# Kernel optimization log

Hardware: AMD Instinct MI355X
Metric: run time of the kernel (lower is better)

Reference implementation:

```python
import jax, jax.numpy as jnp
import numpy as np

N, E, G = 50000, 800000, 100
H, C = 4, 64


def _gatv2(x, src, dst, ea, Wl, bl, Wr, br, We, att, bias):
    # PyG GATv2Conv: x_l = lin_l(x) (source side), x_r = lin_r(x) (target side)
    xl = (x @ Wl + bl).reshape(-1, H, C)
    xr = (x @ Wr + br).reshape(-1, H, C)
    e = (ea @ We).reshape(-1, H, C)               # [E,H,C]
    m = jax.nn.leaky_relu(xl[src] + xr[dst] + e, negative_slope=0.2)
    alpha = jnp.einsum('ehc,hc->eh', m, att)      # [E,H]
    amax = jax.ops.segment_max(alpha, dst, num_segments=N)
    amax = jnp.where(jnp.isfinite(amax), amax, jnp.float32(0.0))
    ex = jnp.exp(alpha - amax[dst])
    denom = jax.ops.segment_sum(ex, dst, num_segments=N)
    a = ex / (denom[dst] + jnp.float32(1e-16))    # segment softmax over in-edges
    out = jax.ops.segment_sum(xl[src] * a[..., None], dst, num_segments=N)
    return out.reshape(N, H * C) + bias


def setup_inputs() -> dict:
    key = jax.random.key(0)
    ks = jax.random.split(key, 24)
    lin = lambda k, i, o: (jax.random.normal(k, (i, o), jnp.float32) / np.sqrt(i).astype(np.float32))
    x = jax.random.normal(ks[0], (N, 8), jnp.float32)
    edge_index = jnp.stack([jax.random.randint(ks[1], (E,), 0, N),
                            jax.random.randint(ks[2], (E,), 0, N)])
    edge_attr = jax.random.normal(ks[3], (E, 1), jnp.float32)
    batch = jnp.sort(jax.random.randint(ks[4], (N,), 0, G))
    return dict(
        x=x, edge_index=edge_index, edge_attr=edge_attr, batch=batch,
        enc_W=lin(ks[5], 8, 64), enc_b=jnp.zeros((64,), jnp.float32),
        g1_Wl=lin(ks[6], 64, 256), g1_bl=jnp.zeros((256,), jnp.float32),
        g1_Wr=lin(ks[7], 64, 256), g1_br=jnp.zeros((256,), jnp.float32),
        g1_We=lin(ks[8], 1, 256),
        g1_att=jax.random.normal(ks[9], (H, C), jnp.float32) / np.sqrt(C).astype(np.float32),
        g1_bias=jnp.zeros((256,), jnp.float32),
        g2_Wl=lin(ks[10], 256, 256), g2_bl=jnp.zeros((256,), jnp.float32),
        g2_Wr=lin(ks[11], 256, 256), g2_br=jnp.zeros((256,), jnp.float32),
        g2_We=lin(ks[12], 1, 256),
        g2_att=jax.random.normal(ks[13], (H, C), jnp.float32) / np.sqrt(C).astype(np.float32),
        g2_bias=jnp.zeros((256,), jnp.float32),
        p1_W=lin(ks[14], 256, 128), p1_b=jnp.zeros((128,), jnp.float32),
        ln_g=jnp.ones((128,), jnp.float32), ln_b=jnp.zeros((128,), jnp.float32),
        p2_W=lin(ks[15], 128, 64), p2_b=jnp.zeros((64,), jnp.float32),
    )


def reference(x, edge_index, edge_attr, batch,
              enc_W, enc_b,
              g1_Wl, g1_bl, g1_Wr, g1_br, g1_We, g1_att, g1_bias,
              g2_Wl, g2_bl, g2_Wr, g2_br, g2_We, g2_att, g2_bias,
              p1_W, p1_b, ln_g, ln_b, p2_W, p2_b):
    src, dst = edge_index[0], edge_index[1]
    h = jax.nn.relu(x @ enc_W + enc_b)
    h = jax.nn.relu(_gatv2(h, src, dst, edge_attr, g1_Wl, g1_bl, g1_Wr, g1_br, g1_We, g1_att, g1_bias))
    h = jax.nn.relu(_gatv2(h, src, dst, edge_attr, g2_Wl, g2_bl, g2_Wr, g2_br, g2_We, g2_att, g2_bias))
    # global mean pool over graphs
    sums = jax.ops.segment_sum(h, batch, num_segments=G)
    cnt = jax.ops.segment_sum(jnp.ones((N, 1), h.dtype), batch, num_segments=G)
    p = sums / jnp.maximum(cnt, jnp.float32(1.0))
    # post MLP (dropout is identity in eval)
    z = p @ p1_W + p1_b
    mu = jnp.mean(z, axis=-1, keepdims=True)
    var = jnp.mean(jnp.square(z - mu), axis=-1, keepdims=True)
    z = (z - mu) * jax.lax.rsqrt(var + jnp.float32(1e-5)) * ln_g + ln_b
    z = jax.nn.relu(z)
    return jax.nn.relu(z @ p2_W + p2_b)
```

## Files before the change

kernel.cpp:

```cpp
#include <hip/hip_runtime.h>

#define NH 4
#define CH 64

__global__ void encoder_kernel(const float* __restrict__ x, const float* __restrict__ W,
                               const float* __restrict__ b, float* __restrict__ h, int N) {
  int idx = blockIdx.x * blockDim.x + threadIdx.x;
  if (idx >= N * 64) return;
  int n = idx >> 6, j = idx & 63;
  const float* xp = x + n * 8;
  float acc = b[j];
#pragma unroll
  for (int k = 0; k < 8; ++k) acc = fmaf(xp[k], W[k * 64 + j], acc);
  h[idx] = fmaxf(acc, 0.0f);
}

template <int K>
__global__ void lin_lr_kernel(const float* __restrict__ h,
                              const float* __restrict__ Wl, const float* __restrict__ bl,
                              const float* __restrict__ Wr, const float* __restrict__ br,
                              float* __restrict__ xl, float* __restrict__ xr, int N) {
  __shared__ float hs[8][K];
  int n0 = blockIdx.x * 8;
  int j = threadIdx.x;
  int nmax = N - n0; if (nmax > 8) nmax = 8;
  for (int idx = j; idx < nmax * K; idx += 256) {
    int m = idx / K, k = idx % K;
    hs[m][k] = h[(size_t)(n0 + m) * K + k];
  }
  __syncthreads();
  float accl[8], accr[8];
  float bjl = bl[j], bjr = br[j];
#pragma unroll
  for (int m = 0; m < 8; ++m) { accl[m] = bjl; accr[m] = bjr; }
  for (int k = 0; k < K; ++k) {
    float wl = Wl[k * 256 + j];
    float wr = Wr[k * 256 + j];
#pragma unroll
    for (int m = 0; m < 8; ++m) {
      accl[m] = fmaf(hs[m][k], wl, accl[m]);
      accr[m] = fmaf(hs[m][k], wr, accr[m]);
    }
  }
  for (int m = 0; m < nmax; ++m) {
    xl[(size_t)(n0 + m) * 256 + j] = accl[m];
    xr[(size_t)(n0 + m) * 256 + j] = accr[m];
  }
}

__global__ void hist_kernel(const int* __restrict__ dst, int* __restrict__ deg, int E) {
  int e = blockIdx.x * blockDim.x + threadIdx.x;
  if (e < E) atomicAdd(&deg[dst[e]], 1);
}

__global__ void scan_partial_kernel(const int* __restrict__ deg, int* __restrict__ partial, int N) {
  __shared__ int sm[256];
  int t = threadIdx.x;
  int i = blockIdx.x * 256 + t;
  sm[t] = (i < N) ? deg[i] : 0;
  __syncthreads();
#pragma unroll
  for (int s = 128; s > 0; s >>= 1) {
    if (t < s) sm[t] += sm[t + s];
    __syncthreads();
  }
  if (t == 0) partial[blockIdx.x] = sm[0];
}

__global__ void scan_offsets_kernel(int* __restrict__ partial, int nb) {
  __shared__ int sm[256];
  int t = threadIdx.x;
  int v = (t < nb) ? partial[t] : 0;
  sm[t] = v;
  __syncthreads();
#pragma unroll
  for (int off = 1; off < 256; off <<= 1) {
    int a = (t >= off) ? sm[t - off] : 0;
    __syncthreads();
    sm[t] += a;
    __syncthreads();
  }
  if (t < nb) partial[t] = sm[t] - v;
}

__global__ void scan_final_kernel(const int* __restrict__ deg, const int* __restrict__ partial,
                                  int* __restrict__ rowptr, int* __restrict__ cursor, int N, int E) {
  __shared__ int sm[256];
  int t = threadIdx.x;
  int i = blockIdx.x * 256 + t;
  int v = (i < N) ? deg[i] : 0;
  sm[t] = v;
  __syncthreads();
#pragma unroll
  for (int off = 1; off < 256; off <<= 1) {
    int a = (t >= off) ? sm[t - off] : 0;
    __syncthreads();
    sm[t] += a;
    __syncthreads();
  }
  if (i < N) {
    int ex = partial[blockIdx.x] + sm[t] - v;
    rowptr[i] = ex;
    cursor[i] = ex;
  }
  if (i == 0) rowptr[N] = E;
}

__global__ void scatter_build_kernel(const int* __restrict__ src, const int* __restrict__ dst,
                                     const float* __restrict__ ea, int* __restrict__ cursor,
                                     int* __restrict__ srcs, float* __restrict__ eas, int E) {
  int e = blockIdx.x * blockDim.x + threadIdx.x;
  if (e >= E) return;
  int d = dst[e];
  int pos = atomicAdd(&cursor[d], 1);
  srcs[pos] = src[e];
  eas[pos] = ea[e];
}

__device__ __forceinline__ void edge_accum(const float4 xlv, const float eav,
                                           const float4 xr4, const float4 We4, const float4 at4,
                                           float4& acc, float& denom) {
  float4 v;
  v.x = fmaf(eav, We4.x, xlv.x + xr4.x);
  v.y = fmaf(eav, We4.y, xlv.y + xr4.y);
  v.z = fmaf(eav, We4.z, xlv.z + xr4.z);
  v.w = fmaf(eav, We4.w, xlv.w + xr4.w);
  v.x = (v.x >= 0.f) ? v.x : 0.2f * v.x;
  v.y = (v.y >= 0.f) ? v.y : 0.2f * v.y;
  v.z = (v.z >= 0.f) ? v.z : 0.2f * v.z;
  v.w = (v.w >= 0.f) ? v.w : 0.2f * v.w;
  float p = v.x * at4.x + v.y * at4.y + v.z * at4.z + v.w * at4.w;
  p += __shfl_xor(p, 1, 64);
  p += __shfl_xor(p, 2, 64);
  p += __shfl_xor(p, 4, 64);
  p += __shfl_xor(p, 8, 64);
  float ex = __expf(p);
  denom += ex;
  acc.x = fmaf(ex, xlv.x, acc.x);
  acc.y = fmaf(ex, xlv.y, acc.y);
  acc.z = fmaf(ex, xlv.z, acc.z);
  acc.w = fmaf(ex, xlv.w, acc.w);
}

template <bool POOL>
__global__ void gat_aggregate_kernel(const int* __restrict__ rowptr,
                                     const int* __restrict__ srcs,
                                     const float* __restrict__ eas,
                                     const float* __restrict__ xl,
                                     const float* __restrict__ xr,
                                     const float* __restrict__ We,
                                     const float* __restrict__ att,
                                     const float* __restrict__ bias,
                                     float* __restrict__ out,
                                     const int* __restrict__ batch,
                                     float* __restrict__ sums,
                                     float* __restrict__ cnt,
                                     int N) {
  int d = (int)((blockIdx.x * (size_t)blockDim.x + threadIdx.x) >> 6);
  int lane = threadIdx.x & 63;
  if (d >= N) return;
  const float4* xl4p = (const float4*)xl;
  float4 xr4 = ((const float4*)xr)[(size_t)d * 64 + lane];
  float4 We4 = ((const float4*)We)[lane];
  float4 at4 = ((const float4*)att)[lane];
  int beg = rowptr[d], end = rowptr[d + 1];
  float4 acc = {0.f, 0.f, 0.f, 0.f};
  float denom = 0.f;
  int i = beg;
  for (; i + 3 < end; i += 4) {
    int s0 = srcs[i], s1 = srcs[i + 1], s2 = srcs[i + 2], s3 = srcs[i + 3];
    float e0 = eas[i], e1 = eas[i + 1], e2 = eas[i + 2], e3 = eas[i + 3];
    float4 a0 = xl4p[(size_t)s0 * 64 + lane];
    float4 a1 = xl4p[(size_t)s1 * 64 + lane];
    float4 a2 = xl4p[(size_t)s2 * 64 + lane];
    float4 a3 = xl4p[(size_t)s3 * 64 + lane];
    edge_accum(a0, e0, xr4, We4, at4, acc, denom);
    edge_accum(a1, e1, xr4, We4, at4, acc, denom);
    edge_accum(a2, e2, xr4, We4, at4, acc, denom);
    edge_accum(a3, e3, xr4, We4, at4, acc, denom);
  }
  for (; i < end; ++i) {
    int s0 = srcs[i];
    float e0 = eas[i];
    float4 a0 = xl4p[(size_t)s0 * 64 + lane];
    edge_accum(a0, e0, xr4, We4, at4, acc, denom);
  }
  float inv = 1.f / (denom + 1e-16f);
  float4 b4 = ((const float4*)bias)[lane];
  float4 o;
  o.x = fmaxf(fmaf(acc.x, inv, b4.x), 0.f);
  o.y = fmaxf(fmaf(acc.y, inv, b4.y), 0.f);
  o.z = fmaxf(fmaf(acc.z, inv, b4.z), 0.f);
  o.w = fmaxf(fmaf(acc.w, inv, b4.w), 0.f);
  if (POOL) {
    int g = batch[d];
    float* sg = sums + (size_t)g * 256 + lane * 4;
    atomicAdd(sg + 0, o.x);
    atomicAdd(sg + 1, o.y);
    atomicAdd(sg + 2, o.z);
    atomicAdd(sg + 3, o.w);
    if (lane == 0) atomicAdd(&cnt[g], 1.0f);
  } else {
    ((float4*)out)[(size_t)d * 64 + lane] = o;
  }
}

__global__ void mlp_kernel(const float* __restrict__ sums, const float* __restrict__ cnt,
                           const float* __restrict__ p1W, const float* __restrict__ p1b,
                           const float* __restrict__ lng, const float* __restrict__ lnb,
                           const float* __restrict__ p2W, const float* __restrict__ p2b,
                           float* __restrict__ outp, int G) {
  __shared__ float p[256];
  __shared__ float z[128];
  __shared__ float wsum[2];
  __shared__ float wsum2[2];
  int g = blockIdx.x;
  int t = threadIdx.x;
  float c = fmaxf(cnt[g], 1.0f);
  p[t] = sums[(size_t)g * 256 + t] / c;
  p[t + 128] = sums[(size_t)g * 256 + t + 128] / c;
  __syncthreads();
  float acc = p1b[t];
  for (int k = 0; k < 256; ++k) acc = fmaf(p[k], p1W[k * 128 + t], acc);
  float v = acc;
#pragma unroll
  for (int off = 32; off > 0; off >>= 1) v += __shfl_xor(v, off, 64);
  if ((t & 63) == 0) wsum[t >> 6] = v;
  __syncthreads();
  float mu = (wsum[0] + wsum[1]) * (1.0f / 128.0f);
  float dv = acc - mu;
  float vv = dv * dv;
#pragma unroll
  for (int off = 32; off > 0; off >>= 1) vv += __shfl_xor(vv, off, 64);
  if ((t & 63) == 0) wsum2[t >> 6] = vv;
  __syncthreads();
  float var = (wsum2[0] + wsum2[1]) * (1.0f / 128.0f);
  float zv = dv * rsqrtf(var + 1e-5f) * lng[t] + lnb[t];
  z[t] = fmaxf(zv, 0.0f);
  __syncthreads();
  if (t < 64) {
    float o = p2b[t];
    for (int k = 0; k < 128; ++k) o = fmaf(z[k], p2W[k * 64 + t], o);
    outp[(size_t)g * 64 + t] = fmaxf(o, 0.0f);
  }
}

extern "C" void kernel_launch(void* const* d_in, const int* in_sizes, int n_in,
                              void* d_out, int out_size, void* d_ws, size_t ws_size,
                              hipStream_t stream) {
  const float* x      = (const float*)d_in[0];
  const int*   ei     = (const int*)d_in[1];
  const float* ea     = (const float*)d_in[2];
  const int*   batch  = (const int*)d_in[3];
  const float* enc_W  = (const float*)d_in[4];
  const float* enc_b  = (const float*)d_in[5];
  const float* Wl1    = (const float*)d_in[6];
  const float* bl1    = (const float*)d_in[7];
  const float* Wr1    = (const float*)d_in[8];
  const float* br1    = (const float*)d_in[9];
  const float* We1    = (const float*)d_in[10];
  const float* att1   = (const float*)d_in[11];
  const float* bias1  = (const float*)d_in[12];
  const float* Wl2    = (const float*)d_in[13];
  const float* bl2    = (const float*)d_in[14];
  const float* Wr2    = (const float*)d_in[15];
  const float* br2    = (const float*)d_in[16];
  const float* We2    = (const float*)d_in[17];
  const float* att2   = (const float*)d_in[18];
  const float* bias2  = (const float*)d_in[19];
  const float* p1W    = (const float*)d_in[20];
  const float* p1b    = (const float*)d_in[21];
  const float* lng    = (const float*)d_in[22];
  const float* lnb    = (const float*)d_in[23];
  const float* p2W    = (const float*)d_in[24];
  const float* p2b    = (const float*)d_in[25];
  float* outp = (float*)d_out;

  int N = in_sizes[0] / 8;
  int E = in_sizes[2];
  int G = out_size / 64;
  const int* src = ei;
  const int* dst = ei + E;
  int nb = (N + 255) / 256;

  float* ws      = (float*)d_ws;
  float* h0      = ws;
  float* B0      = h0     + (size_t)N * 64;
  float* B1      = B0     + (size_t)N * 256;
  float* B2      = B1     + (size_t)N * 256;
  float* eas     = B2     + (size_t)N * 256;
  float* sums    = eas    + (size_t)E;
  float* cnt     = sums   + (size_t)G * 256;
  int*   srcs    = (int*)(cnt + G);
  int*   rowptr  = srcs + (size_t)E;
  int*   cursor  = rowptr + (size_t)(N + 1);
  int*   partial = cursor + (size_t)N;

  encoder_kernel<<<(N * 64 + 255) / 256, 256, 0, stream>>>(x, enc_W, enc_b, h0, N);

  hipMemsetAsync(cursor, 0, (size_t)N * sizeof(int), stream);
  hist_kernel<<<(E + 255) / 256, 256, 0, stream>>>(dst, cursor, E);
  scan_partial_kernel<<<nb, 256, 0, stream>>>(cursor, partial, N);
  scan_offsets_kernel<<<1, 256, 0, stream>>>(partial, nb);
  scan_final_kernel<<<nb, 256, 0, stream>>>(cursor, partial, rowptr, cursor, N, E);
  scatter_build_kernel<<<(E + 255) / 256, 256, 0, stream>>>(src, dst, ea, cursor, srcs, eas, E);

  lin_lr_kernel<64><<<(N + 7) / 8, 256, 0, stream>>>(h0, Wl1, bl1, Wr1, br1, B0, B1, N);
  gat_aggregate_kernel<false><<<(N + 3) / 4, 256, 0, stream>>>(
      rowptr, srcs, eas, B0, B1, We1, att1, bias1, B2, nullptr, nullptr, nullptr, N);

  lin_lr_kernel<256><<<(N + 7) / 8, 256, 0, stream>>>(B2, Wl2, bl2, Wr2, br2, B0, B1, N);
  hipMemsetAsync(sums, 0, ((size_t)G * 256 + G) * sizeof(float), stream);
  gat_aggregate_kernel<true><<<(N + 3) / 4, 256, 0, stream>>>(
      rowptr, srcs, eas, B0, B1, We2, att2, bias2, nullptr, batch, sums, cnt, N);

  mlp_kernel<<<G, 128, 0, stream>>>(sums, cnt, p1W, p1b, lng, lnb, p2W, p2b, outp, G);
}
```

Baseline: 1.039 ms.

## Split GAT aggregation across edges and heads with one block per node

The aggregate kernel now launches one 256-thread block per destination node instead of one wavefront per node. Each wavefront owns one head, and its 64 lanes split into four edge slots of 16 channel lanes each. A node's in-edges are processed 16 at a time with masked tails, and the four slots are combined by cross-lane shuffles before output or pooling. This is meant to expose more parallel gather loads per node and shorten each node's serial edge loop, at the cost of wasted masked lanes on low-degree nodes and an extra shuffle reduction.

```diff
diff --git a/kernel.cpp b/kernel.cpp
--- a/kernel.cpp
+++ b/kernel.cpp
@@ -117,7 +117,7 @@
   eas[pos] = ea[e];
 }
 
-__device__ __forceinline__ void edge_accum(const float4 xlv, const float eav,
+__device__ __forceinline__ void edge_accum(const float4 xlv, const float eav, const float vmask,
                                            const float4 xr4, const float4 We4, const float4 at4,
                                            float4& acc, float& denom) {
   float4 v;
@@ -134,7 +134,7 @@
   p += __shfl_xor(p, 2, 64);
   p += __shfl_xor(p, 4, 64);
   p += __shfl_xor(p, 8, 64);
-  float ex = __expf(p);
+  float ex = __expf(p) * vmask;
   denom += ex;
   acc.x = fmaf(ex, xlv.x, acc.x);
   acc.y = fmaf(ex, xlv.y, acc.y);
@@ -156,52 +156,67 @@
                                      float* __restrict__ sums,
                                      float* __restrict__ cnt,
                                      int N) {
-  int d = (int)((blockIdx.x * (size_t)blockDim.x + threadIdx.x) >> 6);
+  int d = blockIdx.x;
+  int h = threadIdx.x >> 6;
   int lane = threadIdx.x & 63;
-  if (d >= N) return;
+  int es = lane >> 4;
+  int ch = lane & 15;
   const float4* xl4p = (const float4*)xl;
-  float4 xr4 = ((const float4*)xr)[(size_t)d * 64 + lane];
-  float4 We4 = ((const float4*)We)[lane];
-  float4 at4 = ((const float4*)att)[lane];
+  int hb = h * 16 + ch;
+  float4 xr4 = ((const float4*)xr)[(size_t)d * 64 + hb];
+  float4 We4 = ((const float4*)We)[hb];
+  float4 at4 = ((const float4*)att)[hb];
   int beg = rowptr[d], end = rowptr[d + 1];
   float4 acc = {0.f, 0.f, 0.f, 0.f};
   float denom = 0.f;
-  int i = beg;
-  for (; i + 3 < end; i += 4) {
-    int s0 = srcs[i], s1 = srcs[i + 1], s2 = srcs[i + 2], s3 = srcs[i + 3];
-    float e0 = eas[i], e1 = eas[i + 1], e2 = eas[i + 2], e3 = eas[i + 3];
-    float4 a0 = xl4p[(size_t)s0 * 64 + lane];
-    float4 a1 = xl4p[(size_t)s1 * 64 + lane];
-    float4 a2 = xl4p[(size_t)s2 * 64 + lane];
-    float4 a3 = xl4p[(size_t)s3 * 64 + lane];
-    edge_accum(a0, e0, xr4, We4, at4, acc, denom);
-    edge_accum(a1, e1, xr4, We4, at4, acc, denom);
-    edge_accum(a2, e2, xr4, We4, at4, acc, denom);
-    edge_accum(a3, e3, xr4, We4, at4, acc, denom);
-  }
-  for (; i < end; ++i) {
-    int s0 = srcs[i];
-    float e0 = eas[i];
-    float4 a0 = xl4p[(size_t)s0 * 64 + lane];
-    edge_accum(a0, e0, xr4, We4, at4, acc, denom);
-  }
-  float inv = 1.f / (denom + 1e-16f);
-  float4 b4 = ((const float4*)bias)[lane];
-  float4 o;
-  o.x = fmaxf(fmaf(acc.x, inv, b4.x), 0.f);
-  o.y = fmaxf(fmaf(acc.y, inv, b4.y), 0.f);
-  o.z = fmaxf(fmaf(acc.z, inv, b4.z), 0.f);
-  o.w = fmaxf(fmaf(acc.w, inv, b4.w), 0.f);
-  if (POOL) {
-    int g = batch[d];
-    float* sg = sums + (size_t)g * 256 + lane * 4;
-    atomicAdd(sg + 0, o.x);
-    atomicAdd(sg + 1, o.y);
-    atomicAdd(sg + 2, o.z);
-    atomicAdd(sg + 3, o.w);
-    if (lane == 0) atomicAdd(&cnt[g], 1.0f);
-  } else {
-    ((float4*)out)[(size_t)d * 64 + lane] = o;
+  for (int i = beg; i < end; i += 16) {
+    int i0 = i + es, i1 = i + 4 + es, i2 = i + 8 + es, i3 = i + 12 + es;
+    float m0 = (i0 < end) ? 1.f : 0.f;
+    float m1 = (i1 < end) ? 1.f : 0.f;
+    float m2 = (i2 < end) ? 1.f : 0.f;
+    float m3 = (i3 < end) ? 1.f : 0.f;
+    int c0 = (i0 < end) ? i0 : end - 1;
+    int c1 = (i1 < end) ? i1 : end - 1;
+    int c2 = (i2 < end) ? i2 : end - 1;
+    int c3 = (i3 < end) ? i3 : end - 1;
+    int s0 = srcs[c0], s1 = srcs[c1], s2 = srcs[c2], s3 = srcs[c3];
+    float e0 = eas[c0], e1 = eas[c1], e2 = eas[c2], e3 = eas[c3];
+    float4 a0 = xl4p[(size_t)s0 * 64 + hb];
+    float4 a1 = xl4p[(size_t)s1 * 64 + hb];
+    float4 a2 = xl4p[(size_t)s2 * 64 + hb];
+    float4 a3 = xl4p[(size_t)s3 * 64 + hb];
+    edge_accum(a0, e0, m0, xr4, We4, at4, acc, denom);
+    edge_accum(a1, e1, m1, xr4, We4, at4, acc, denom);
+    edge_accum(a2, e2, m2, xr4, We4, at4, acc, denom);
+    edge_accum(a3, e3, m3, xr4, We4, at4, acc, denom);
+  }
+#pragma unroll
+  for (int off = 16; off <= 32; off <<= 1) {
+    denom += __shfl_xor(denom, off, 64);
+    acc.x += __shfl_xor(acc.x, off, 64);
+    acc.y += __shfl_xor(acc.y, off, 64);
+    acc.z += __shfl_xor(acc.z, off, 64);
+    acc.w += __shfl_xor(acc.w, off, 64);
+  }
+  if (lane < 16) {
+    float inv = 1.f / (denom + 1e-16f);
+    float4 b4 = ((const float4*)bias)[hb];
+    float4 o;
+    o.x = fmaxf(fmaf(acc.x, inv, b4.x), 0.f);
+    o.y = fmaxf(fmaf(acc.y, inv, b4.y), 0.f);
+    o.z = fmaxf(fmaf(acc.z, inv, b4.z), 0.f);
+    o.w = fmaxf(fmaf(acc.w, inv, b4.w), 0.f);
+    if (POOL) {
+      int g = batch[d];
+      float* sg = sums + (size_t)g * 256 + hb * 4;
+      atomicAdd(sg + 0, o.x);
+      atomicAdd(sg + 1, o.y);
+      atomicAdd(sg + 2, o.z);
+      atomicAdd(sg + 3, o.w);
+      if (lane == 0 && h == 0) atomicAdd(&cnt[g], 1.0f);
+    } else {
+      ((float4*)out)[(size_t)d * 64 + hb] = o;
+    }
   }
 }
 
@@ -306,12 +321,12 @@
   scatter_build_kernel<<<(E + 255) / 256, 256, 0, stream>>>(src, dst, ea, cursor, srcs, eas, E);
 
   lin_lr_kernel<64><<<(N + 7) / 8, 256, 0, stream>>>(h0, Wl1, bl1, Wr1, br1, B0, B1, N);
-  gat_aggregate_kernel<false><<<(N + 3) / 4, 256, 0, stream>>>(
+  gat_aggregate_kernel<false><<<N, 256, 0, stream>>>(
       rowptr, srcs, eas, B0, B1, We1, att1, bias1, B2, nullptr, nullptr, nullptr, N);
 
   lin_lr_kernel<256><<<(N + 7) / 8, 256, 0, stream>>>(B2, Wl2, bl2, Wr2, br2, B0, B1, N);
   hipMemsetAsync(sums, 0, ((size_t)G * 256 + G) * sizeof(float), stream);
-  gat_aggregate_kernel<true><<<(N + 3) / 4, 256, 0, stream>>>(
+  gat_aggregate_kernel<true><<<N, 256, 0, stream>>>(
       rowptr, srcs, eas, B0, B1, We2, att2, bias2, nullptr, batch, sums, cnt, N);
 
   mlp_kernel<<<G, 128, 0, stream>>>(sums, cnt, p1W, p1b, lng, lnb, p2W, p2b, outp, G);
```

Result: slower. 1.165 ms (+12.1%).

## Store source-side features in fp16 and deepen edge gather unrolling to eight

Applied to the files above, without the earlier changes.

The lin_l output is now written as fp16, and the aggregation kernel gathers it as packed half2 pairs that it converts to fp32 before the attention math. This halves the bytes moved by the random per-edge gathers that dominate the aggregation kernels. The main edge loop is also unrolled to 8 edges so more gathers are in flight at once. The cost is reduced precision in both the attention logits and the aggregated messages, plus higher register pressure from the deeper unroll.

```diff
diff --git a/kernel.cpp b/kernel.cpp
--- a/kernel.cpp
+++ b/kernel.cpp
@@ -1,4 +1,5 @@
 #include <hip/hip_runtime.h>
+#include <hip/hip_fp16.h>
 
 #define NH 4
 #define CH 64
@@ -19,7 +20,7 @@
 __global__ void lin_lr_kernel(const float* __restrict__ h,
                               const float* __restrict__ Wl, const float* __restrict__ bl,
                               const float* __restrict__ Wr, const float* __restrict__ br,
-                              float* __restrict__ xl, float* __restrict__ xr, int N) {
+                              __half* __restrict__ xl, float* __restrict__ xr, int N) {
   __shared__ float hs[8][K];
   int n0 = blockIdx.x * 8;
   int j = threadIdx.x;
@@ -43,7 +44,7 @@
     }
   }
   for (int m = 0; m < nmax; ++m) {
-    xl[(size_t)(n0 + m) * 256 + j] = accl[m];
+    xl[(size_t)(n0 + m) * 256 + j] = __float2half_rn(accl[m]);
     xr[(size_t)(n0 + m) * 256 + j] = accr[m];
   }
 }
@@ -115,6 +116,15 @@
   int pos = atomicAdd(&cursor[d], 1);
   srcs[pos] = src[e];
   eas[pos] = ea[e];
+}
+
+__device__ __forceinline__ float4 ldxl(const uint2* __restrict__ xlh, int s, int lane) {
+  uint2 r = xlh[(size_t)s * 64 + lane];
+  __half2 a = *reinterpret_cast<const __half2*>(&r.x);
+  __half2 b = *reinterpret_cast<const __half2*>(&r.y);
+  float2 fa = __half22float2(a);
+  float2 fb = __half22float2(b);
+  return make_float4(fa.x, fa.y, fb.x, fb.y);
 }
 
 __device__ __forceinline__ void edge_accum(const float4 xlv, const float eav,
@@ -146,7 +156,7 @@
 __global__ void gat_aggregate_kernel(const int* __restrict__ rowptr,
                                      const int* __restrict__ srcs,
                                      const float* __restrict__ eas,
-                                     const float* __restrict__ xl,
+                                     const __half* __restrict__ xl,
                                      const float* __restrict__ xr,
                                      const float* __restrict__ We,
                                      const float* __restrict__ att,
@@ -159,7 +169,7 @@
   int d = (int)((blockIdx.x * (size_t)blockDim.x + threadIdx.x) >> 6);
   int lane = threadIdx.x & 63;
   if (d >= N) return;
-  const float4* xl4p = (const float4*)xl;
+  const uint2* xlh = (const uint2*)xl;
   float4 xr4 = ((const float4*)xr)[(size_t)d * 64 + lane];
   float4 We4 = ((const float4*)We)[lane];
   float4 at4 = ((const float4*)att)[lane];
@@ -167,23 +177,29 @@
   float4 acc = {0.f, 0.f, 0.f, 0.f};
   float denom = 0.f;
   int i = beg;
+  for (; i + 7 < end; i += 8) {
+    int s[8]; float ev[8];
+#pragma unroll
+    for (int k = 0; k < 8; ++k) { s[k] = srcs[i + k]; ev[k] = eas[i + k]; }
+    float4 a[8];
+#pragma unroll
+    for (int k = 0; k < 8; ++k) a[k] = ldxl(xlh, s[k], lane);
+#pragma unroll
+    for (int k = 0; k < 8; ++k) edge_accum(a[k], ev[k], xr4, We4, at4, acc, denom);
+  }
   for (; i + 3 < end; i += 4) {
-    int s0 = srcs[i], s1 = srcs[i + 1], s2 = srcs[i + 2], s3 = srcs[i + 3];
-    float e0 = eas[i], e1 = eas[i + 1], e2 = eas[i + 2], e3 = eas[i + 3];
-    float4 a0 = xl4p[(size_t)s0 * 64 + lane];
-    float4 a1 = xl4p[(size_t)s1 * 64 + lane];
-    float4 a2 = xl4p[(size_t)s2 * 64 + lane];
-    float4 a3 = xl4p[(size_t)s3 * 64 + lane];
-    edge_accum(a0, e0, xr4, We4, at4, acc, denom);
-    edge_accum(a1, e1, xr4, We4, at4, acc, denom);
-    edge_accum(a2, e2, xr4, We4, at4, acc, denom);
-    edge_accum(a3, e3, xr4, We4, at4, acc, denom);
+    int s[4]; float ev[4];
+#pragma unroll
+    for (int k = 0; k < 4; ++k) { s[k] = srcs[i + k]; ev[k] = eas[i + k]; }
+    float4 a[4];
+#pragma unroll
+    for (int k = 0; k < 4; ++k) a[k] = ldxl(xlh, s[k], lane);
+#pragma unroll
+    for (int k = 0; k < 4; ++k) edge_accum(a[k], ev[k], xr4, We4, at4, acc, denom);
   }
   for (; i < end; ++i) {
-    int s0 = srcs[i];
-    float e0 = eas[i];
-    float4 a0 = xl4p[(size_t)s0 * 64 + lane];
-    edge_accum(a0, e0, xr4, We4, at4, acc, denom);
+    float4 a0 = ldxl(xlh, srcs[i], lane);
+    edge_accum(a0, eas[i], xr4, We4, at4, acc, denom);
   }
   float inv = 1.f / (denom + 1e-16f);
   float4 b4 = ((const float4*)bias)[lane];
@@ -295,6 +311,7 @@
   int*   rowptr  = srcs + (size_t)E;
   int*   cursor  = rowptr + (size_t)(N + 1);
   int*   partial = cursor + (size_t)N;
+  __half* B0h    = (__half*)B0;
 
   encoder_kernel<<<(N * 64 + 255) / 256, 256, 0, stream>>>(x, enc_W, enc_b, h0, N);
 
@@ -305,14 +322,14 @@
   scan_final_kernel<<<nb, 256, 0, stream>>>(cursor, partial, rowptr, cursor, N, E);
   scatter_build_kernel<<<(E + 255) / 256, 256, 0, stream>>>(src, dst, ea, cursor, srcs, eas, E);
 
-  lin_lr_kernel<64><<<(N + 7) / 8, 256, 0, stream>>>(h0, Wl1, bl1, Wr1, br1, B0, B1, N);
+  lin_lr_kernel<64><<<(N + 7) / 8, 256, 0, stream>>>(h0, Wl1, bl1, Wr1, br1, B0h, B1, N);
   gat_aggregate_kernel<false><<<(N + 3) / 4, 256, 0, stream>>>(
-      rowptr, srcs, eas, B0, B1, We1, att1, bias1, B2, nullptr, nullptr, nullptr, N);
-
-  lin_lr_kernel<256><<<(N + 7) / 8, 256, 0, stream>>>(B2, Wl2, bl2, Wr2, br2, B0, B1, N);
+      rowptr, srcs, eas, B0h, B1, We1, att1, bias1, B2, nullptr, nullptr, nullptr, N);
+
+  lin_lr_kernel<256><<<(N + 7) / 8, 256, 0, stream>>>(B2, Wl2, bl2, Wr2, br2, B0h, B1, N);
   hipMemsetAsync(sums, 0, ((size_t)G * 256 + G) * sizeof(float), stream);
   gat_aggregate_kernel<true><<<(N + 3) / 4, 256, 0, stream>>>(
-      rowptr, srcs, eas, B0, B1, We2, att2, bias2, nullptr, batch, sums, cnt, N);
+      rowptr, srcs, eas, B0h, B1, We2, att2, bias2, nullptr, batch, sums, cnt, N);
 
   mlp_kernel<<<G, 128, 0, stream>>>(sums, cnt, p1W, p1b, lng, lnb, p2W, p2b, outp, G);
 }
```

New measurement: 1.077 ms. 3.7% more time.
